# Optimization experiments

Hardware: AMD Instinct MI355X
Metric: run time of the kernel (lower is better)

The kernel has to match this reference:

```python
import jax, jax.numpy as jnp
import numpy as np

B, N, CQ, H, CH = 1, 256, 128, 4, 32  # batch, n_res, c_q(=c_k=c_v), heads, per-head dim


def setup_inputs() -> dict:
    key = jax.random.key(0)
    ks = jax.random.split(key, 12)
    s = 0.02
    q_x = jax.random.normal(ks[0], (B, N, N, CQ), jnp.float32)
    kv_x = jax.random.normal(ks[1], (B, N, N, CQ), jnp.float32)
    # mask bias: 0 where kept, -1e9 where masked (additive mask)
    keep = jax.random.uniform(ks[2], (B, N, 1, 1, N)) < 0.9
    mask_bias = jnp.where(keep, 0.0, -1e9).astype(jnp.float32)
    triangle_bias = jax.random.normal(ks[3], (B, 1, H, N, N), jnp.float32)
    # projection weights, stored per-head as [H, CH, C_in]
    wq = jax.random.normal(ks[4], (H, CH, CQ), jnp.float32) * s
    wk = jax.random.normal(ks[5], (H, CH, CQ), jnp.float32) * s
    wv = jax.random.normal(ks[6], (H, CH, CQ), jnp.float32) * s
    wg = jax.random.normal(ks[7], (H, CH, CQ), jnp.float32) * s
    bg = jax.random.normal(ks[8], (H, CH), jnp.float32) * s + 1.0  # gating bias init 1
    wo = jax.random.normal(ks[9], (CQ, H * CH), jnp.float32) * s
    bo = jnp.zeros((CQ,), jnp.float32)
    return {"q_x": q_x, "kv_x": kv_x, "mask_bias": mask_bias,
            "triangle_bias": triangle_bias, "wq": wq, "wk": wk, "wv": wv,
            "wg": wg, "bg": bg, "wo": wo, "bo": bo}


def reference(q_x, kv_x, mask_bias, triangle_bias, wq, wk, wv, wg, bg, wo, bo):
    scale = 1.0 / np.sqrt(CH).astype(np.float32)
    # project + split heads: [B,N,Q,C] x [H,D,C] -> [B,N,H,Q,D]
    q = jnp.einsum('bnqc,hdc->bnhqd', q_x, wq) * scale
    k = jnp.einsum('bnkc,hdc->bnhkd', kv_x, wk)
    v = jnp.einsum('bnkc,hdc->bnhkd', kv_x, wv)
    # scores + additive biases (mask_bias broadcasts over h,q; triangle over n)
    a = jnp.einsum('bnhqd,bnhkd->bnhqk', q, k) + mask_bias + triangle_bias
    a = jax.nn.softmax(a, axis=-1)
    o = jnp.einsum('bnhqk,bnhkd->bnhqd', a, v)
    o = jnp.swapaxes(o, -2, -3)  # [B,N,Q,H,D]
    # gating
    g = jax.nn.sigmoid(jnp.einsum('bnqc,hdc->bnqhd', q_x, wg) + bg)
    o = o * g
    o = o.reshape(o.shape[:-2] + (H * CH,))  # [B,N,Q,H*D]
    return jnp.einsum('bnqe,ce->bnqc', o, wo) + bo
```

## Files before the change

kernel.cpp:

```cpp
#include <hip/hip_runtime.h>

#define NRES 256
#define CIN  128
#define NH   4
#define DH   32

typedef __attribute__((ext_vector_type(4))) float f32x4;
typedef __attribute__((ext_vector_type(8))) short bf16x8;
typedef unsigned short u16;

#define U_WQG 0
#define U_WKV 32768
#define U_WWO 65536
#define U_QB  131072
#define U_KB  (U_QB + 8388608)
#define U_VT  (U_KB + 8388608)
#define U_GB  (U_VT + 8388608)
#define WS_NEED ((size_t)(U_GB + 8388608) * 2)

__device__ __forceinline__ unsigned pkbf(float a, float b) {
    unsigned ua = __builtin_bit_cast(unsigned, a);
    unsigned ub = __builtin_bit_cast(unsigned, b);
    ua += 0x7fffu + ((ua >> 16) & 1u);
    ub += 0x7fffu + ((ub >> 16) & 1u);
    return __builtin_amdgcn_perm(ub, ua, 0x07060302);
}
__device__ __forceinline__ u16 f2bfu(float f) {
    unsigned u = __builtin_bit_cast(unsigned, f);
    return (u16)((u + 0x7fffu + ((u >> 16) & 1u)) >> 16);
}
__device__ __forceinline__ float bf2f(u16 v) {
    unsigned u = ((unsigned)v) << 16;
    return __builtin_bit_cast(float, u);
}
union bfr { unsigned u[4]; bf16x8 v; };
__device__ __forceinline__ bf16x8 ldcvt8(const float* __restrict__ p) {
    f32x4 a = *(const f32x4*)p; f32x4 b = *(const f32x4*)(p + 4);
    bfr r;
    r.u[0] = pkbf(a[0], a[1]); r.u[1] = pkbf(a[2], a[3]);
    r.u[2] = pkbf(b[0], b[1]); r.u[3] = pkbf(b[2], b[3]);
    return r.v;
}
__device__ __forceinline__ bf16x8 ldcvt8s(const float* __restrict__ p, float sc) {
    f32x4 a = *(const f32x4*)p; f32x4 b = *(const f32x4*)(p + 4);
    bfr r;
    r.u[0] = pkbf(a[0] * sc, a[1] * sc); r.u[1] = pkbf(a[2] * sc, a[3] * sc);
    r.u[2] = pkbf(b[0] * sc, b[1] * sc); r.u[3] = pkbf(b[2] * sc, b[3] * sc);
    return r.v;
}
#define MFMA(a, b, c) __builtin_amdgcn_mfma_f32_16x16x32_bf16((a), (b), (c), 0, 0, 0)

__global__ void wconv(const float* __restrict__ wq, const float* __restrict__ wk,
                      const float* __restrict__ wv, const float* __restrict__ wg,
                      const float* __restrict__ wo, u16* __restrict__ ws)
{
    const int i0 = (blockIdx.x * 256 + threadIdx.x) * 8;
    const float qsc = 0.17677669529663687f;
    const float* src; u16* dst; float sc = 1.f;
    if (i0 < 32768) {
        const int e = i0 >> 7, c = i0 & 127;
        src = (e < 128 ? wq + e * CIN : wg + (e - 128) * CIN) + c;
        if (e < 128) sc = qsc;
        dst = ws + U_WQG + i0;
    } else if (i0 < 65536) {
        const int j = i0 - 32768, e = j >> 7, c = j & 127;
        src = (e < 128 ? wk + e * CIN : wv + (e - 128) * CIN) + c;
        dst = ws + U_WKV + j;
    } else {
        const int j = i0 - 65536;
        src = wo + j; dst = ws + U_WWO + j;
    }
    *(bf16x8*)dst = ldcvt8s(src, sc);
}

__global__ __launch_bounds__(256, 4) void proj(
    const float* __restrict__ q_x, const float* __restrict__ kv_x,
    const float* __restrict__ bg, u16* __restrict__ ws)
{
    const int t = threadIdx.x, lane = t & 63, w = t >> 6;
    const int mrow = lane & 15, grp = lane >> 4;
    const int koff = grp * 8, rbase = grp * 4;
    const int R0 = blockIdx.x * 64 + w * 16;
    const int ysel = blockIdx.y;
    const float* __restrict__ src = ysel ? kv_x : q_x;
    const u16* __restrict__ W = ws + (ysel ? U_WKV : U_WQG);

    const f32x4 zf = {0.f, 0.f, 0.f, 0.f};
    f32x4 acc[16];
    #pragma unroll
    for (int nt = 0; nt < 16; ++nt) acc[nt] = zf;

    #pragma unroll
    for (int ct = 0; ct < 4; ++ct) {
        const int c0 = ct * 32 + koff;
        bf16x8 aX = ldcvt8(src + (size_t)(R0 + mrow) * CIN + c0);
        #pragma unroll
        for (int nt = 0; nt < 16; ++nt) {
            bf16x8 bw = *(const bf16x8*)(W + (nt * 16 + mrow) * CIN + c0);
            acc[nt] = MFMA(aX, bw, acc[nt]);
        }
    }

    if (!ysel) {
        #pragma unroll
        for (int nt = 0; nt < 8; ++nt) {
            const int e = nt * 16 + mrow;
            #pragma unroll
            for (int r = 0; r < 4; ++r)
                ws[U_QB + (size_t)(R0 + rbase + r) * CIN + e] = f2bfu(acc[nt][r]);
        }
        #pragma unroll
        for (int nt = 8; nt < 16; ++nt) {
            const int e = (nt - 8) * 16 + mrow;
            const float b = bg[e];
            #pragma unroll
            for (int r = 0; r < 4; ++r) {
                const float g = 1.f / (1.f + __expf(-(acc[nt][r] + b)));
                ws[U_GB + (size_t)(R0 + rbase + r) * CIN + e] = f2bfu(g);
            }
        }
    } else {
        #pragma unroll
        for (int nt = 0; nt < 8; ++nt) {
            const int e = nt * 16 + mrow;
            #pragma unroll
            for (int r = 0; r < 4; ++r)
                ws[U_KB + (size_t)(R0 + rbase + r) * CIN + e] = f2bfu(acc[nt][r]);
        }
        const int n = R0 >> 8, k0 = (R0 & 255) + rbase;
        #pragma unroll
        for (int nt = 8; nt < 16; ++nt) {
            const int dcol = (nt - 8) * 16 + mrow;
            uint2 v;
            v.x = pkbf(acc[nt][0], acc[nt][1]);
            v.y = pkbf(acc[nt][2], acc[nt][3]);
            *(uint2*)&ws[U_VT + ((size_t)n * 128 + dcol) * 256 + k0] = v;
        }
    }
}

#define PST 40
__global__ __launch_bounds__(256, 4) void flash(
    const u16* __restrict__ ws, const float* __restrict__ mask_bias,
    const float* __restrict__ tri_bias, float* __restrict__ o_out)
{
    const int h = blockIdx.x, n = blockIdx.y;
    const int t = threadIdx.x, lane = t & 63, w = t >> 6;
    const int mrow = lane & 15, grp = lane >> 4;
    const int koff = grp * 8, rbase = grp * 4;
    const int q0 = w * 64;

    __shared__ u16 Pt[4 * 64 * PST];
    __shared__ float msk[NRES];

    if (t < 64) *(float4*)&msk[t * 4] = *(const float4*)(mask_bias + n * NRES + t * 4);

    const u16* __restrict__ Qb = ws + U_QB + (size_t)n * NRES * CIN;
    const u16* __restrict__ Kb = ws + U_KB + (size_t)n * NRES * CIN;
    const u16* __restrict__ Vt = ws + U_VT + (size_t)n * 128 * 256;
    const u16* __restrict__ Gb = ws + U_GB + (size_t)n * NRES * CIN;
    const float* __restrict__ trih = tri_bias + (size_t)h * NRES * NRES;

    bf16x8 aq[4];
    #pragma unroll
    for (int qt = 0; qt < 4; ++qt)
        aq[qt] = *(const bf16x8*)(Qb + (size_t)(q0 + qt * 16 + mrow) * CIN + h * DH + koff);
    __syncthreads();

    const f32x4 zf = {0.f, 0.f, 0.f, 0.f};
    f32x4 oa[4][2], ls4[4];
    #pragma unroll
    for (int qt = 0; qt < 4; ++qt) { oa[qt][0] = zf; oa[qt][1] = zf; ls4[qt] = zf; }

    u16* __restrict__ pw = &Pt[w * 64 * PST];

    for (int kt = 0; kt < 8; ++kt) {
        const int kb = kt * 32;
        bf16x8 bk0 = *(const bf16x8*)(Kb + (size_t)(kb + mrow) * CIN + h * DH + koff);
        bf16x8 bk1 = *(const bf16x8*)(Kb + (size_t)(kb + 16 + mrow) * CIN + h * DH + koff);
        bf16x8 bv0 = *(const bf16x8*)(Vt + (size_t)(h * DH + mrow) * NRES + kb + koff);
        bf16x8 bv1 = *(const bf16x8*)(Vt + (size_t)(h * DH + 16 + mrow) * NRES + kb + koff);
        const float mb0 = msk[kb + mrow] - 8.f;
        const float mb1 = msk[kb + 16 + mrow] - 8.f;

        #pragma unroll
        for (int h2 = 0; h2 < 2; ++h2) {
            float tr0[2][4], tr1[2][4];
            #pragma unroll
            for (int j = 0; j < 2; ++j) {
                const int qt = h2 * 2 + j;
                const float* __restrict__ trow =
                    trih + (q0 + qt * 16 + rbase) * NRES + kb + mrow;
                #pragma unroll
                for (int r = 0; r < 4; ++r) {
                    tr0[j][r] = trow[r * NRES];
                    tr1[j][r] = trow[r * NRES + 16];
                }
            }
            #pragma unroll
            for (int j = 0; j < 2; ++j) {
                const int qt = h2 * 2 + j;
                f32x4 s0 = MFMA(aq[qt], bk0, zf);
                f32x4 s1 = MFMA(aq[qt], bk1, zf);
                #pragma unroll
                for (int r = 0; r < 4; ++r) {
                    s0[r] = __expf(s0[r] + tr0[j][r] + mb0);
                    s1[r] = __expf(s1[r] + tr1[j][r] + mb1);
                }
                ls4[qt] += s0 + s1;
                #pragma unroll
                for (int r = 0; r < 4; ++r) {
                    pw[(qt * 16 + rbase + r) * PST + mrow]      = f2bfu(s0[r]);
                    pw[(qt * 16 + rbase + r) * PST + 16 + mrow] = f2bfu(s1[r]);
                }
            }
        }
        asm volatile("s_waitcnt lgkmcnt(0)" ::: "memory");
        #pragma unroll
        for (int qt = 0; qt < 4; ++qt) {
            bf16x8 pa = *(const bf16x8*)&pw[(qt * 16 + mrow) * PST + koff];
            oa[qt][0] = MFMA(pa, bv0, oa[qt][0]);
            oa[qt][1] = MFMA(pa, bv1, oa[qt][1]);
        }
    }

    float* __restrict__ orow = o_out + (size_t)n * NRES * CIN + h * DH;
    #pragma unroll
    for (int qt = 0; qt < 4; ++qt) {
        f32x4 lv = ls4[qt];
        #pragma unroll
        for (int xm = 1; xm < 16; xm <<= 1) {
            lv[0] += __shfl_xor(lv[0], xm, 64);
            lv[1] += __shfl_xor(lv[1], xm, 64);
            lv[2] += __shfl_xor(lv[2], xm, 64);
            lv[3] += __shfl_xor(lv[3], xm, 64);
        }
        #pragma unroll
        for (int r = 0; r < 4; ++r) {
            const float inv = 1.f / lv[r];
            const int q = q0 + qt * 16 + rbase + r;
            const float g0 = bf2f(Gb[(size_t)q * CIN + h * DH + mrow]);
            const float g1 = bf2f(Gb[(size_t)q * CIN + h * DH + 16 + mrow]);
            orow[q * CIN + mrow]      = oa[qt][0][r] * inv * g0;
            orow[q * CIN + 16 + mrow] = oa[qt][1][r] * inv * g1;
        }
    }
}

__global__ __launch_bounds__(256, 4) void gout(
    const u16* __restrict__ ws, const float* __restrict__ bo, float* io)
{
    const int t = threadIdx.x, lane = t & 63, w = t >> 6;
    const int mrow = lane & 15, grp = lane >> 4;
    const int koff = grp * 8, rbase = grp * 4;
    const int r0 = blockIdx.x * 128 + w * 32;
    const u16* __restrict__ Wo = ws + U_WWO;

    const f32x4 zf = {0.f, 0.f, 0.f, 0.f};
    f32x4 acc[2][8];
    #pragma unroll
    for (int at = 0; at < 2; ++at)
        #pragma unroll
        for (int nt = 0; nt < 8; ++nt) acc[at][nt] = zf;

    #pragma unroll
    for (int ks = 0; ks < 4; ++ks) {
        const int e0 = ks * 32 + koff;
        bf16x8 a0 = ldcvt8(io + (size_t)(r0 + mrow) * CIN + e0);
        bf16x8 a1 = ldcvt8(io + (size_t)(r0 + 16 + mrow) * CIN + e0);
        #pragma unroll
        for (int nt = 0; nt < 8; ++nt) {
            bf16x8 bw = *(const bf16x8*)(Wo + (nt * 16 + mrow) * CIN + e0);
            acc[0][nt] = MFMA(a0, bw, acc[0][nt]);
            acc[1][nt] = MFMA(a1, bw, acc[1][nt]);
        }
    }

    #pragma unroll
    for (int nt = 0; nt < 8; ++nt) {
        const float bc = bo[nt * 16 + mrow];
        #pragma unroll
        for (int at = 0; at < 2; ++at)
            #pragma unroll
            for (int r = 0; r < 4; ++r)
                io[(size_t)(r0 + at * 16 + rbase + r) * CIN + nt * 16 + mrow] =
                    acc[at][nt][r] + bc;
    }
}

#define KST 32
#define VST 264
#define GST 136

__global__ __launch_bounds__(256, 3) void attn_fb(
    const float* __restrict__ q_x, const float* __restrict__ kv_x,
    const float* __restrict__ mask_bias, const float* __restrict__ tri_bias,
    const float* __restrict__ wq, const float* __restrict__ wk,
    const float* __restrict__ wv, float* __restrict__ o_out)
{
    const int h = blockIdx.x, n = blockIdx.y;
    const int t = threadIdx.x;
    const int lane = t & 63, w = t >> 6;
    const int mrow = lane & 15;
    const int grp  = lane >> 4;
    const int koff = grp * 8;
    const int rbase = grp * 4;
    const int q0 = w * 64;

    __shared__ u16 Ks[NRES * KST];
    __shared__ u16 Vt[DH * VST];
    __shared__ u16 Ptb[4 * 32 * PST];
    __shared__ float msk[NRES];

    if (t < 64) *(float4*)&msk[t * 4] = *(const float4*)(mask_bias + n * NRES + t * 4);

    const float* __restrict__ qxn = q_x  + (size_t)n * NRES * CIN;
    const float* __restrict__ kxn = kv_x + (size_t)n * NRES * CIN;
    const float* __restrict__ wqh = wq + h * DH * CIN;
    const float* __restrict__ wkh = wk + h * DH * CIN;
    const float* __restrict__ wvh = wv + h * DH * CIN;

    f32x4 aq_[4][2], ak_[4][2], av_[4][2];
    const f32x4 zf = {0.f, 0.f, 0.f, 0.f};
    #pragma unroll
    for (int qt = 0; qt < 4; ++qt)
        #pragma unroll
        for (int dt = 0; dt < 2; ++dt) { aq_[qt][dt] = zf; ak_[qt][dt] = zf; av_[qt][dt] = zf; }

    const float qsc = 0.17677669529663687f;
    #pragma unroll
    for (int ct = 0; ct < 4; ++ct) {
        const int c0 = ct * 32 + koff;
        bf16x8 bq0 = ldcvt8s(wqh + mrow * CIN + c0, qsc);
        bf16x8 bq1 = ldcvt8s(wqh + (16 + mrow) * CIN + c0, qsc);
        bf16x8 bk0 = ldcvt8(wkh + mrow * CIN + c0);
        bf16x8 bk1 = ldcvt8(wkh + (16 + mrow) * CIN + c0);
        bf16x8 bv0 = ldcvt8(wvh + mrow * CIN + c0);
        bf16x8 bv1 = ldcvt8(wvh + (16 + mrow) * CIN + c0);
        #pragma unroll
        for (int qt = 0; qt < 4; ++qt) {
            bf16x8 aX = ldcvt8(qxn + (q0 + qt * 16 + mrow) * CIN + c0);
            aq_[qt][0] = MFMA(aX, bq0, aq_[qt][0]);
            aq_[qt][1] = MFMA(aX, bq1, aq_[qt][1]);
            bf16x8 aK = ldcvt8(kxn + (q0 + qt * 16 + mrow) * CIN + c0);
            ak_[qt][0] = MFMA(aK, bk0, ak_[qt][0]);
            ak_[qt][1] = MFMA(aK, bk1, ak_[qt][1]);
            av_[qt][0] = MFMA(aK, bv0, av_[qt][0]);
            av_[qt][1] = MFMA(aK, bv1, av_[qt][1]);
        }
    }

    #pragma unroll
    for (int qt = 0; qt < 4; ++qt)
        #pragma unroll
        for (int dt = 0; dt < 2; ++dt)
            #pragma unroll
            for (int r = 0; r < 4; ++r) {
                const int row = q0 + qt * 16 + rbase + r;
                const int d = dt * 16 + mrow;
                Ks[row * KST + d] = f2bfu(ak_[qt][dt][r]);
                Vt[d * VST + row] = f2bfu(av_[qt][dt][r]);
            }

    u16* __restrict__ pw = &Ptb[w * 32 * PST];
    bf16x8 aq[4];
    #pragma unroll
    for (int h2 = 0; h2 < 2; ++h2) {
        #pragma unroll
        for (int j = 0; j < 2; ++j) {
            const int qt = h2 * 2 + j;
            #pragma unroll
            for (int dt = 0; dt < 2; ++dt)
                #pragma unroll
                for (int r = 0; r < 4; ++r)
                    pw[(j * 16 + rbase + r) * PST + dt * 16 + mrow] = f2bfu(aq_[qt][dt][r]);
        }
        asm volatile("s_waitcnt lgkmcnt(0)" ::: "memory");
        #pragma unroll
        for (int j = 0; j < 2; ++j)
            aq[h2 * 2 + j] = *(const bf16x8*)&pw[(j * 16 + mrow) * PST + koff];
        asm volatile("s_waitcnt lgkmcnt(0)" ::: "memory");
    }
    __syncthreads();

    f32x4 oa[4][2], ls4[4];
    #pragma unroll
    for (int qt = 0; qt < 4; ++qt) { oa[qt][0] = zf; oa[qt][1] = zf; ls4[qt] = zf; }

    const float* __restrict__ trih = tri_bias + (size_t)h * NRES * NRES;

    for (int kt = 0; kt < 8; ++kt) {
        const int kb = kt * 32;
        bf16x8 bk0 = *(const bf16x8*)&Ks[(kb + mrow) * KST + koff];
        bf16x8 bk1 = *(const bf16x8*)&Ks[(kb + 16 + mrow) * KST + koff];
        bf16x8 bv0 = *(const bf16x8*)&Vt[mrow * VST + kb + koff];
        bf16x8 bv1 = *(const bf16x8*)&Vt[(16 + mrow) * VST + kb + koff];
        const float mb0 = msk[kb + mrow] - 8.f;
        const float mb1 = msk[kb + 16 + mrow] - 8.f;

        #pragma unroll
        for (int h2 = 0; h2 < 2; ++h2) {
            float tr0[2][4], tr1[2][4];
            #pragma unroll
            for (int j = 0; j < 2; ++j) {
                const int qt = h2 * 2 + j;
                const float* __restrict__ trow =
                    trih + (q0 + qt * 16 + rbase) * NRES + kb + mrow;
                #pragma unroll
                for (int r = 0; r < 4; ++r) {
                    tr0[j][r] = trow[r * NRES];
                    tr1[j][r] = trow[r * NRES + 16];
                }
            }
            #pragma unroll
            for (int j = 0; j < 2; ++j) {
                const int qt = h2 * 2 + j;
                f32x4 s0 = MFMA(aq[qt], bk0, zf);
                f32x4 s1 = MFMA(aq[qt], bk1, zf);
                #pragma unroll
                for (int r = 0; r < 4; ++r) {
                    s0[r] = __expf(s0[r] + tr0[j][r] + mb0);
                    s1[r] = __expf(s1[r] + tr1[j][r] + mb1);
                }
                ls4[qt] += s0 + s1;
                #pragma unroll
                for (int r = 0; r < 4; ++r) {
                    pw[(j * 16 + rbase + r) * PST + mrow]      = f2bfu(s0[r]);
                    pw[(j * 16 + rbase + r) * PST + 16 + mrow] = f2bfu(s1[r]);
                }
            }
            asm volatile("s_waitcnt lgkmcnt(0)" ::: "memory");
            #pragma unroll
            for (int j = 0; j < 2; ++j) {
                const int qt = h2 * 2 + j;
                bf16x8 pa = *(const bf16x8*)&pw[(j * 16 + mrow) * PST + koff];
                oa[qt][0] = MFMA(pa, bv0, oa[qt][0]);
                oa[qt][1] = MFMA(pa, bv1, oa[qt][1]);
            }
        }
    }

    float* __restrict__ orow = o_out + (size_t)n * NRES * CIN + h * DH;
    #pragma unroll
    for (int qt = 0; qt < 4; ++qt) {
        f32x4 lv = ls4[qt];
        #pragma unroll
        for (int xm = 1; xm < 16; xm <<= 1) {
            lv[0] += __shfl_xor(lv[0], xm, 64);
            lv[1] += __shfl_xor(lv[1], xm, 64);
            lv[2] += __shfl_xor(lv[2], xm, 64);
            lv[3] += __shfl_xor(lv[3], xm, 64);
        }
        #pragma unroll
        for (int r = 0; r < 4; ++r) {
            const float inv = 1.f / lv[r];
            const int q = q0 + qt * 16 + rbase + r;
            orow[q * CIN + mrow]      = oa[qt][0][r] * inv;
            orow[q * CIN + 16 + mrow] = oa[qt][1][r] * inv;
        }
    }
}

__global__ __launch_bounds__(256, 4) void gate_fb(
    const float* __restrict__ q_x, const float* __restrict__ wg,
    const float* __restrict__ bg, const float* __restrict__ wo,
    const float* __restrict__ bo, float* io)
{
    const int t = threadIdx.x;
    const int lane = t & 63, w = t >> 6;
    const int mrow = lane & 15, grp = lane >> 4;
    const int koff = grp * 8, rbase = grp * 4;
    const int r0 = blockIdx.x * 128 + w * 32;

    __shared__ u16 Gt[4 * 32 * GST];
    u16* __restrict__ gw = &Gt[w * 32 * GST];

    const f32x4 zf = {0.f, 0.f, 0.f, 0.f};
    f32x4 acc[2][8];
    #pragma unroll
    for (int at = 0; at < 2; ++at)
        #pragma unroll
        for (int nt = 0; nt < 8; ++nt) acc[at][nt] = zf;

    #pragma unroll
    for (int ks = 0; ks < 4; ++ks) {
        const int c0 = ks * 32 + koff;
        bf16x8 ax0 = ldcvt8(q_x + (size_t)(r0 + mrow) * CIN + c0);
        bf16x8 ax1 = ldcvt8(q_x + (size_t)(r0 + 16 + mrow) * CIN + c0);
        #pragma unroll
        for (int nt = 0; nt < 8; ++nt) {
            bf16x8 bw = ldcvt8(wg + (nt * 16 + mrow) * CIN + c0);
            acc[0][nt] = MFMA(ax0, bw, acc[0][nt]);
            acc[1][nt] = MFMA(ax1, bw, acc[1][nt]);
        }
    }

    #pragma unroll
    for (int nt = 0; nt < 8; ++nt) {
        const float bge = bg[nt * 16 + mrow];
        #pragma unroll
        for (int at = 0; at < 2; ++at)
            #pragma unroll
            for (int r = 0; r < 4; ++r) {
                const int qg = r0 + at * 16 + rbase + r;
                const float ov = io[(size_t)qg * CIN + nt * 16 + mrow];
                const float g = 1.f / (1.f + __expf(-(acc[at][nt][r] + bge)));
                gw[(at * 16 + rbase + r) * GST + nt * 16 + mrow] = f2bfu(ov * g);
            }
    }
    asm volatile("s_waitcnt lgkmcnt(0)" ::: "memory");

    f32x4 acc2[2][8];
    #pragma unroll
    for (int at = 0; at < 2; ++at)
        #pragma unroll
        for (int nt = 0; nt < 8; ++nt) acc2[at][nt] = zf;

    #pragma unroll
    for (int ks = 0; ks < 4; ++ks) {
        const int e0 = ks * 32 + koff;
        bf16x8 ag0 = *(const bf16x8*)&gw[mrow * GST + e0];
        bf16x8 ag1 = *(const bf16x8*)&gw[(16 + mrow) * GST + e0];
        #pragma unroll
        for (int nt = 0; nt < 8; ++nt) {
            bf16x8 bw = ldcvt8(wo + (nt * 16 + mrow) * CIN + e0);
            acc2[0][nt] = MFMA(ag0, bw, acc2[0][nt]);
            acc2[1][nt] = MFMA(ag1, bw, acc2[1][nt]);
        }
    }

    #pragma unroll
    for (int nt = 0; nt < 8; ++nt) {
        const float boc = bo[nt * 16 + mrow];
        #pragma unroll
        for (int at = 0; at < 2; ++at)
            #pragma unroll
            for (int r = 0; r < 4; ++r)
                io[(size_t)(r0 + at * 16 + rbase + r) * CIN + nt * 16 + mrow] =
                    acc2[at][nt][r] + boc;
    }
}

extern "C" void kernel_launch(void* const* d_in, const int* in_sizes, int n_in,
                              void* d_out, int out_size, void* d_ws, size_t ws_size,
                              hipStream_t stream) {
    const float* q_x  = (const float*)d_in[0];
    const float* kv_x = (const float*)d_in[1];
    const float* mask = (const float*)d_in[2];
    const float* tri  = (const float*)d_in[3];
    const float* wq   = (const float*)d_in[4];
    const float* wk   = (const float*)d_in[5];
    const float* wv   = (const float*)d_in[6];
    const float* wg   = (const float*)d_in[7];
    const float* bg   = (const float*)d_in[8];
    const float* wo   = (const float*)d_in[9];
    const float* bo   = (const float*)d_in[10];
    float* out = (float*)d_out;

    if (ws_size >= WS_NEED) {
        u16* ws16 = (u16*)d_ws;
        wconv<<<40, 256, 0, stream>>>(wq, wk, wv, wg, wo, ws16);
        proj<<<dim3(1024, 2), 256, 0, stream>>>(q_x, kv_x, bg, ws16);
        flash<<<dim3(NH, NRES), 256, 0, stream>>>(ws16, mask, tri, out);
        gout<<<512, 256, 0, stream>>>(ws16, bo, out);
    } else {
        attn_fb<<<dim3(NH, NRES), 256, 0, stream>>>(q_x, kv_x, mask, tri, wq, wk, wv, out);
        gate_fb<<<(NRES * NRES) / 128, 256, 0, stream>>>(q_x, wg, bg, wo, bo, out);
    }
}
```

Baseline: 246.2 us.

## Stage activation tiles in LDS and compute transposed scores in flash

The proj and gout kernels now stage a block of fp32 activation rows into shared memory as bf16 with coalesced 16-element loads. Warps then split output columns (proj) or rows (gout) instead of each converting its own rows from global memory, and grid sizes double to match. The flash kernel computes S^T (K as the A operand, Q as B) so each lane reads the triangle bias and mask as contiguous float4 vectors and writes P with packed uint2 stores. The row-sum reduction is also simplified to two shuffles. These changes add an LDS stage and barrier per block in proj and gout.

```diff
diff --git a/kernel.cpp b/kernel.cpp
--- a/kernel.cpp
+++ b/kernel.cpp
@@ -47,6 +47,17 @@
     r.u[0] = pkbf(a[0] * sc, a[1] * sc); r.u[1] = pkbf(a[2] * sc, a[3] * sc);
     r.u[2] = pkbf(b[0] * sc, b[1] * sc); r.u[3] = pkbf(b[2] * sc, b[3] * sc);
     return r.v;
+}
+__device__ __forceinline__ void stage16(const float* __restrict__ p, u16* dst) {
+    f32x4 a = *(const f32x4*)p,     b = *(const f32x4*)(p + 4);
+    f32x4 c = *(const f32x4*)(p + 8), d = *(const f32x4*)(p + 12);
+    bfr x, y;
+    x.u[0] = pkbf(a[0], a[1]); x.u[1] = pkbf(a[2], a[3]);
+    x.u[2] = pkbf(b[0], b[1]); x.u[3] = pkbf(b[2], b[3]);
+    y.u[0] = pkbf(c[0], c[1]); y.u[1] = pkbf(c[2], c[3]);
+    y.u[2] = pkbf(d[0], d[1]); y.u[3] = pkbf(d[2], d[3]);
+    *(bf16x8*)dst = x.v;
+    *(bf16x8*)(dst + 8) = y.v;
 }
 #define MFMA(a, b, c) __builtin_amdgcn_mfma_f32_16x16x32_bf16((a), (b), (c), 0, 0, 0)
 
@@ -73,6 +84,7 @@
     *(bf16x8*)dst = ldcvt8s(src, sc);
 }
 
+#define XST 136
 __global__ __launch_bounds__(256, 4) void proj(
     const float* __restrict__ q_x, const float* __restrict__ kv_x,
     const float* __restrict__ bg, u16* __restrict__ ws)
@@ -80,61 +92,94 @@
     const int t = threadIdx.x, lane = t & 63, w = t >> 6;
     const int mrow = lane & 15, grp = lane >> 4;
     const int koff = grp * 8, rbase = grp * 4;
-    const int R0 = blockIdx.x * 64 + w * 16;
+    const int R0 = blockIdx.x * 32;
     const int ysel = blockIdx.y;
     const float* __restrict__ src = ysel ? kv_x : q_x;
     const u16* __restrict__ W = ws + (ysel ? U_WKV : U_WQG);
 
+    __shared__ u16 Xs[32 * XST];
+
+    {
+        const int row = t >> 3, c0 = (t & 7) * 16;
+        stage16(src + (size_t)(R0 + row) * CIN + c0, &Xs[row * XST + c0]);
+    }
+    __syncthreads();
+
+    const int cb = w * 64;
+    const u16* __restrict__ Wc = W + (size_t)cb * CIN;
+
     const f32x4 zf = {0.f, 0.f, 0.f, 0.f};
-    f32x4 acc[16];
-    #pragma unroll
-    for (int nt = 0; nt < 16; ++nt) acc[nt] = zf;
+    f32x4 acc[2][4];
+    #pragma unroll
+    for (int rt = 0; rt < 2; ++rt)
+        #pragma unroll
+        for (int nt = 0; nt < 4; ++nt) acc[rt][nt] = zf;
 
     #pragma unroll
     for (int ct = 0; ct < 4; ++ct) {
         const int c0 = ct * 32 + koff;
-        bf16x8 aX = ldcvt8(src + (size_t)(R0 + mrow) * CIN + c0);
-        #pragma unroll
-        for (int nt = 0; nt < 16; ++nt) {
-            bf16x8 bw = *(const bf16x8*)(W + (nt * 16 + mrow) * CIN + c0);
-            acc[nt] = MFMA(aX, bw, acc[nt]);
+        bf16x8 a0 = *(const bf16x8*)&Xs[mrow * XST + c0];
+        bf16x8 a1 = *(const bf16x8*)&Xs[(16 + mrow) * XST + c0];
+        #pragma unroll
+        for (int nt = 0; nt < 4; ++nt) {
+            bf16x8 bw = *(const bf16x8*)(Wc + (size_t)(nt * 16 + mrow) * CIN + c0);
+            acc[0][nt] = MFMA(a0, bw, acc[0][nt]);
+            acc[1][nt] = MFMA(a1, bw, acc[1][nt]);
         }
     }
 
     if (!ysel) {
-        #pragma unroll
-        for (int nt = 0; nt < 8; ++nt) {
-            const int e = nt * 16 + mrow;
-            #pragma unroll
-            for (int r = 0; r < 4; ++r)
-                ws[U_QB + (size_t)(R0 + rbase + r) * CIN + e] = f2bfu(acc[nt][r]);
-        }
-        #pragma unroll
-        for (int nt = 8; nt < 16; ++nt) {
-            const int e = (nt - 8) * 16 + mrow;
-            const float b = bg[e];
-            #pragma unroll
-            for (int r = 0; r < 4; ++r) {
-                const float g = 1.f / (1.f + __expf(-(acc[nt][r] + b)));
-                ws[U_GB + (size_t)(R0 + rbase + r) * CIN + e] = f2bfu(g);
+        if (cb < 128) {
+            #pragma unroll
+            for (int nt = 0; nt < 4; ++nt) {
+                const int e = cb + nt * 16 + mrow;
+                #pragma unroll
+                for (int rt = 0; rt < 2; ++rt)
+                    #pragma unroll
+                    for (int r = 0; r < 4; ++r)
+                        ws[U_QB + (size_t)(R0 + rt * 16 + rbase + r) * CIN + e] =
+                            f2bfu(acc[rt][nt][r]);
+            }
+        } else {
+            #pragma unroll
+            for (int nt = 0; nt < 4; ++nt) {
+                const int e = cb - 128 + nt * 16 + mrow;
+                const float b = bg[e];
+                #pragma unroll
+                for (int rt = 0; rt < 2; ++rt)
+                    #pragma unroll
+                    for (int r = 0; r < 4; ++r) {
+                        const float g = 1.f / (1.f + __expf(-(acc[rt][nt][r] + b)));
+                        ws[U_GB + (size_t)(R0 + rt * 16 + rbase + r) * CIN + e] = f2bfu(g);
+                    }
             }
         }
     } else {
-        #pragma unroll
-        for (int nt = 0; nt < 8; ++nt) {
-            const int e = nt * 16 + mrow;
-            #pragma unroll
-            for (int r = 0; r < 4; ++r)
-                ws[U_KB + (size_t)(R0 + rbase + r) * CIN + e] = f2bfu(acc[nt][r]);
-        }
-        const int n = R0 >> 8, k0 = (R0 & 255) + rbase;
-        #pragma unroll
-        for (int nt = 8; nt < 16; ++nt) {
-            const int dcol = (nt - 8) * 16 + mrow;
-            uint2 v;
-            v.x = pkbf(acc[nt][0], acc[nt][1]);
-            v.y = pkbf(acc[nt][2], acc[nt][3]);
-            *(uint2*)&ws[U_VT + ((size_t)n * 128 + dcol) * 256 + k0] = v;
+        if (cb < 128) {
+            #pragma unroll
+            for (int nt = 0; nt < 4; ++nt) {
+                const int e = cb + nt * 16 + mrow;
+                #pragma unroll
+                for (int rt = 0; rt < 2; ++rt)
+                    #pragma unroll
+                    for (int r = 0; r < 4; ++r)
+                        ws[U_KB + (size_t)(R0 + rt * 16 + rbase + r) * CIN + e] =
+                            f2bfu(acc[rt][nt][r]);
+            }
+        } else {
+            const int n = R0 >> 8;
+            #pragma unroll
+            for (int nt = 0; nt < 4; ++nt) {
+                const int d = cb - 128 + nt * 16 + mrow;
+                #pragma unroll
+                for (int rt = 0; rt < 2; ++rt) {
+                    const int k0 = (R0 & 255) + rt * 16 + rbase;
+                    uint2 v;
+                    v.x = pkbf(acc[rt][nt][0], acc[rt][nt][1]);
+                    v.y = pkbf(acc[rt][nt][2], acc[rt][nt][3]);
+                    *(uint2*)&ws[U_VT + ((size_t)n * 128 + d) * 256 + k0] = v;
+                }
+            }
         }
     }
 }
@@ -161,59 +206,50 @@
     const u16* __restrict__ Gb = ws + U_GB + (size_t)n * NRES * CIN;
     const float* __restrict__ trih = tri_bias + (size_t)h * NRES * NRES;
 
-    bf16x8 aq[4];
+    bf16x8 bq[4];
     #pragma unroll
     for (int qt = 0; qt < 4; ++qt)
-        aq[qt] = *(const bf16x8*)(Qb + (size_t)(q0 + qt * 16 + mrow) * CIN + h * DH + koff);
+        bq[qt] = *(const bf16x8*)(Qb + (size_t)(q0 + qt * 16 + mrow) * CIN + h * DH + koff);
     __syncthreads();
 
     const f32x4 zf = {0.f, 0.f, 0.f, 0.f};
-    f32x4 oa[4][2], ls4[4];
-    #pragma unroll
-    for (int qt = 0; qt < 4; ++qt) { oa[qt][0] = zf; oa[qt][1] = zf; ls4[qt] = zf; }
+    f32x4 oa[4][2];
+    float ls[4] = {0.f, 0.f, 0.f, 0.f};
+    #pragma unroll
+    for (int qt = 0; qt < 4; ++qt) { oa[qt][0] = zf; oa[qt][1] = zf; }
 
     u16* __restrict__ pw = &Pt[w * 64 * PST];
 
     for (int kt = 0; kt < 8; ++kt) {
         const int kb = kt * 32;
-        bf16x8 bk0 = *(const bf16x8*)(Kb + (size_t)(kb + mrow) * CIN + h * DH + koff);
-        bf16x8 bk1 = *(const bf16x8*)(Kb + (size_t)(kb + 16 + mrow) * CIN + h * DH + koff);
+        bf16x8 ak0 = *(const bf16x8*)(Kb + (size_t)(kb + mrow) * CIN + h * DH + koff);
+        bf16x8 ak1 = *(const bf16x8*)(Kb + (size_t)(kb + 16 + mrow) * CIN + h * DH + koff);
         bf16x8 bv0 = *(const bf16x8*)(Vt + (size_t)(h * DH + mrow) * NRES + kb + koff);
         bf16x8 bv1 = *(const bf16x8*)(Vt + (size_t)(h * DH + 16 + mrow) * NRES + kb + koff);
-        const float mb0 = msk[kb + mrow] - 8.f;
-        const float mb1 = msk[kb + 16 + mrow] - 8.f;
-
-        #pragma unroll
-        for (int h2 = 0; h2 < 2; ++h2) {
-            float tr0[2][4], tr1[2][4];
-            #pragma unroll
-            for (int j = 0; j < 2; ++j) {
-                const int qt = h2 * 2 + j;
-                const float* __restrict__ trow =
-                    trih + (q0 + qt * 16 + rbase) * NRES + kb + mrow;
-                #pragma unroll
-                for (int r = 0; r < 4; ++r) {
-                    tr0[j][r] = trow[r * NRES];
-                    tr1[j][r] = trow[r * NRES + 16];
-                }
-            }
-            #pragma unroll
-            for (int j = 0; j < 2; ++j) {
-                const int qt = h2 * 2 + j;
-                f32x4 s0 = MFMA(aq[qt], bk0, zf);
-                f32x4 s1 = MFMA(aq[qt], bk1, zf);
-                #pragma unroll
-                for (int r = 0; r < 4; ++r) {
-                    s0[r] = __expf(s0[r] + tr0[j][r] + mb0);
-                    s1[r] = __expf(s1[r] + tr1[j][r] + mb1);
-                }
-                ls4[qt] += s0 + s1;
-                #pragma unroll
-                for (int r = 0; r < 4; ++r) {
-                    pw[(qt * 16 + rbase + r) * PST + mrow]      = f2bfu(s0[r]);
-                    pw[(qt * 16 + rbase + r) * PST + 16 + mrow] = f2bfu(s1[r]);
-                }
-            }
+        f32x4 mk0 = *(const f32x4*)&msk[kb + rbase];
+        f32x4 mk1 = *(const f32x4*)&msk[kb + 16 + rbase];
+        #pragma unroll
+        for (int r = 0; r < 4; ++r) { mk0[r] -= 8.f; mk1[r] -= 8.f; }
+
+        #pragma unroll
+        for (int qt = 0; qt < 4; ++qt) {
+            f32x4 s0 = MFMA(ak0, bq[qt], zf);
+            f32x4 s1 = MFMA(ak1, bq[qt], zf);
+            const float* __restrict__ tq =
+                trih + (size_t)(q0 + qt * 16 + mrow) * NRES + kb + rbase;
+            f32x4 t0 = *(const f32x4*)tq;
+            f32x4 t1 = *(const f32x4*)(tq + 16);
+            #pragma unroll
+            for (int r = 0; r < 4; ++r) {
+                s0[r] = __expf(s0[r] + t0[r] + mk0[r]);
+                s1[r] = __expf(s1[r] + t1[r] + mk1[r]);
+            }
+            ls[qt] += s0[0] + s0[1] + s0[2] + s0[3] + s1[0] + s1[1] + s1[2] + s1[3];
+            uint2 p0, p1;
+            p0.x = pkbf(s0[0], s0[1]); p0.y = pkbf(s0[2], s0[3]);
+            p1.x = pkbf(s1[0], s1[1]); p1.y = pkbf(s1[2], s1[3]);
+            *(uint2*)&pw[(qt * 16 + mrow) * PST + rbase] = p0;
+            *(uint2*)&pw[(qt * 16 + mrow) * PST + 16 + rbase] = p1;
         }
         asm volatile("s_waitcnt lgkmcnt(0)" ::: "memory");
         #pragma unroll
@@ -227,22 +263,18 @@
     float* __restrict__ orow = o_out + (size_t)n * NRES * CIN + h * DH;
     #pragma unroll
     for (int qt = 0; qt < 4; ++qt) {
-        f32x4 lv = ls4[qt];
-        #pragma unroll
-        for (int xm = 1; xm < 16; xm <<= 1) {
-            lv[0] += __shfl_xor(lv[0], xm, 64);
-            lv[1] += __shfl_xor(lv[1], xm, 64);
-            lv[2] += __shfl_xor(lv[2], xm, 64);
-            lv[3] += __shfl_xor(lv[3], xm, 64);
-        }
+        float lred = ls[qt];
+        lred += __shfl_xor(lred, 16, 64);
+        lred += __shfl_xor(lred, 32, 64);
+        const float linv = 1.f / lred;
         #pragma unroll
         for (int r = 0; r < 4; ++r) {
-            const float inv = 1.f / lv[r];
+            const float iv = __shfl(linv, rbase + r, 64);
             const int q = q0 + qt * 16 + rbase + r;
             const float g0 = bf2f(Gb[(size_t)q * CIN + h * DH + mrow]);
             const float g1 = bf2f(Gb[(size_t)q * CIN + h * DH + 16 + mrow]);
-            orow[q * CIN + mrow]      = oa[qt][0][r] * inv * g0;
-            orow[q * CIN + 16 + mrow] = oa[qt][1][r] * inv * g1;
+            orow[q * CIN + mrow]      = oa[qt][0][r] * iv * g0;
+            orow[q * CIN + 16 + mrow] = oa[qt][1][r] * iv * g1;
         }
     }
 }
@@ -253,26 +285,33 @@
     const int t = threadIdx.x, lane = t & 63, w = t >> 6;
     const int mrow = lane & 15, grp = lane >> 4;
     const int koff = grp * 8, rbase = grp * 4;
-    const int r0 = blockIdx.x * 128 + w * 32;
+    const int r0 = blockIdx.x * 64;
     const u16* __restrict__ Wo = ws + U_WWO;
 
+    __shared__ u16 Xs[64 * XST];
+
+    {
+        const int row = t >> 2, c0 = (t & 3) * 32;
+        const float* p = io + (size_t)(r0 + row) * CIN + c0;
+        stage16(p,      &Xs[row * XST + c0]);
+        stage16(p + 16, &Xs[row * XST + c0 + 16]);
+    }
+    __syncthreads();
+
+    const int rw = w * 16;
     const f32x4 zf = {0.f, 0.f, 0.f, 0.f};
-    f32x4 acc[2][8];
-    #pragma unroll
-    for (int at = 0; at < 2; ++at)
-        #pragma unroll
-        for (int nt = 0; nt < 8; ++nt) acc[at][nt] = zf;
-
-    #pragma unroll
-    for (int ks = 0; ks < 4; ++ks) {
-        const int e0 = ks * 32 + koff;
-        bf16x8 a0 = ldcvt8(io + (size_t)(r0 + mrow) * CIN + e0);
-        bf16x8 a1 = ldcvt8(io + (size_t)(r0 + 16 + mrow) * CIN + e0);
+    f32x4 acc[8];
+    #pragma unroll
+    for (int nt = 0; nt < 8; ++nt) acc[nt] = zf;
+
+    #pragma unroll
+    for (int ct = 0; ct < 4; ++ct) {
+        const int c0 = ct * 32 + koff;
+        bf16x8 a0 = *(const bf16x8*)&Xs[(rw + mrow) * XST + c0];
         #pragma unroll
         for (int nt = 0; nt < 8; ++nt) {
-            bf16x8 bw = *(const bf16x8*)(Wo + (nt * 16 + mrow) * CIN + e0);
-            acc[0][nt] = MFMA(a0, bw, acc[0][nt]);
-            acc[1][nt] = MFMA(a1, bw, acc[1][nt]);
+            bf16x8 bw = *(const bf16x8*)(Wo + (size_t)(nt * 16 + mrow) * CIN + c0);
+            acc[nt] = MFMA(a0, bw, acc[nt]);
         }
     }
 
@@ -280,11 +319,8 @@
     for (int nt = 0; nt < 8; ++nt) {
         const float bc = bo[nt * 16 + mrow];
         #pragma unroll
-        for (int at = 0; at < 2; ++at)
-            #pragma unroll
-            for (int r = 0; r < 4; ++r)
-                io[(size_t)(r0 + at * 16 + rbase + r) * CIN + nt * 16 + mrow] =
-                    acc[at][nt][r] + bc;
+        for (int r = 0; r < 4; ++r)
+            io[(size_t)(r0 + rw + rbase + r) * CIN + nt * 16 + mrow] = acc[nt][r] + bc;
     }
 }
 
@@ -560,9 +596,9 @@
     if (ws_size >= WS_NEED) {
         u16* ws16 = (u16*)d_ws;
         wconv<<<40, 256, 0, stream>>>(wq, wk, wv, wg, wo, ws16);
-        proj<<<dim3(1024, 2), 256, 0, stream>>>(q_x, kv_x, bg, ws16);
+        proj<<<dim3(2048, 2), 256, 0, stream>>>(q_x, kv_x, bg, ws16);
         flash<<<dim3(NH, NRES), 256, 0, stream>>>(ws16, mask, tri, out);
-        gout<<<512, 256, 0, stream>>>(ws16, bo, out);
+        gout<<<1024, 256, 0, stream>>>(ws16, bo, out);
     } else {
         attn_fb<<<dim3(NH, NRES), 256, 0, stream>>>(q_x, kv_x, mask, tri, wq, wk, wv, out);
         gate_fb<<<(NRES * NRES) / 128, 256, 0, stream>>>(q_x, wg, bg, wo, bo, out);
```

Measured after the change: 246.4 us. No clear change (+0.1%).
